# Optimization experiments

Hardware: AMD Instinct MI355X
Metric: run time of the kernel (lower is better)

## Reference

```python
import jax, jax.numpy as jnp
import numpy as np

D_MODEL = 1024
N_HEADS = 16
D_FF = 4096
B, T = 4, 2048
EPS = 1e-5


def layernorm(x, g, b):
    mu = jnp.mean(x, axis=-1, keepdims=True)
    var = jnp.var(x, axis=-1, keepdims=True)
    return (x - mu) * jax.lax.rsqrt(var + EPS) * g + b


def setup_inputs() -> dict:
    key = jax.random.key(0)
    ks = jax.random.split(key, 8)
    s = 0.02
    return {
        "x": jax.random.normal(ks[0], (B, T, D_MODEL), jnp.float32),
        "ln1_g": jnp.ones((D_MODEL,), jnp.float32),
        "ln1_b": jnp.zeros((D_MODEL,), jnp.float32),
        "wq": jax.random.normal(ks[1], (D_MODEL, D_MODEL), jnp.float32) * s,
        "bq": jnp.zeros((D_MODEL,), jnp.float32),
        "wk": jax.random.normal(ks[2], (D_MODEL, D_MODEL), jnp.float32) * s,
        "bk": jnp.zeros((D_MODEL,), jnp.float32),
        "wv": jax.random.normal(ks[3], (D_MODEL, D_MODEL), jnp.float32) * s,
        "bv": jnp.zeros((D_MODEL,), jnp.float32),
        "wo": jax.random.normal(ks[4], (D_MODEL, D_MODEL), jnp.float32) * s,
        "bo": jnp.zeros((D_MODEL,), jnp.float32),
        "ln2_g": jnp.ones((D_MODEL,), jnp.float32),
        "ln2_b": jnp.zeros((D_MODEL,), jnp.float32),
        "w1": jax.random.normal(ks[5], (D_FF, D_MODEL), jnp.float32) * s,
        "b1": jnp.zeros((D_FF,), jnp.float32),
        "w2": jax.random.normal(ks[6], (D_MODEL, D_FF), jnp.float32) * s,
        "b2": jnp.zeros((D_MODEL,), jnp.float32),
    }


def reference(x, ln1_g, ln1_b, wq, bq, wk, bk, wv, bv, wo, bo,
              ln2_g, ln2_b, w1, b1, w2, b2):
    d_k = D_MODEL // N_HEADS
    # --- attention sublayer (pre-LN) ---
    h = layernorm(x, ln1_g, ln1_b)                       # [B,T,D]
    q = (h @ wq.T + bq).reshape(B, T, N_HEADS, d_k)
    k = (h @ wk.T + bk).reshape(B, T, N_HEADS, d_k)
    v = (h @ wv.T + bv).reshape(B, T, N_HEADS, d_k)
    scores = jnp.einsum("bqhd,bkhd->bhqk", q, k) / jnp.sqrt(jnp.float32(d_k))
    attn = jax.nn.softmax(scores, axis=-1)               # [B,H,T,T]
    o = jnp.einsum("bhqk,bkhd->bqhd", attn, v).reshape(B, T, D_MODEL)
    x = x + (o @ wo.T + bo)
    # --- FFN sublayer ---
    h2 = layernorm(x, ln2_g, ln2_b)
    h2 = jax.nn.gelu(h2 @ w1.T + b1, approximate=False)  # torch GELU = exact erf
    x = x + (h2 @ w2.T + b2)
    return x
```

## Files before the change

### kernel.cpp

```cpp
#include <hip/hip_runtime.h>
#include <math.h>


#define D_MODEL 1024
#define D_FF    4096
#define NH      16
#define BATCH   4
#define SEQ     2048
#define DK      64
#define MTOK    (BATCH*SEQ)
#define NBH     (BATCH*NH)

typedef __bf16 bf16;
typedef _Float16 f16;
typedef bf16  bf16x4 __attribute__((ext_vector_type(4)));
typedef bf16  bf16x8 __attribute__((ext_vector_type(8)));
typedef f16   f16x4  __attribute__((ext_vector_type(4)));
typedef f16   f16x8  __attribute__((ext_vector_type(8)));
typedef __fp16 hf16x2 __attribute__((ext_vector_type(2)));
typedef __fp16 hf16x4 __attribute__((ext_vector_type(4)));
typedef __fp16 hf16x8 __attribute__((ext_vector_type(8)));
typedef float f32x4  __attribute__((ext_vector_type(4)));

__device__ __forceinline__ void gload_lds16(const void* g, void* l) {
  __builtin_amdgcn_global_load_lds(
      (__attribute__((address_space(1))) void*)g,
      (__attribute__((address_space(3))) void*)l, 16, 0, 0);
}

#define BAR() __builtin_amdgcn_s_barrier()
#define WAIT_VM0() do { asm volatile("s_waitcnt vmcnt(0)" ::: "memory"); \
  __builtin_amdgcn_sched_barrier(0); } while (0)

__device__ __forceinline__ float gelu_fast(float x) {
  float ax = fabsf(x) * 0.70710678118654752f;
  float t  = 1.0f / (1.0f + 0.3275911f * ax);
  float p  = t * (0.254829592f + t * (-0.284496736f + t * (1.421413741f +
             t * (-1.453152027f + t * 1.061405429f))));
  float e  = __builtin_amdgcn_exp2f(ax * ax * -1.4426950408889634f);
  float er = 1.0f - p * e;
  er = __builtin_copysignf(er, x);
  return 0.5f * x * (1.0f + er);
}

__global__ __launch_bounds__(256) void cast_w(const float* __restrict__ s,
                                              bf16* __restrict__ d, int n) {
  int i = (blockIdx.x * 256 + threadIdx.x) * 4;
  if (i >= n) return;
  float4 v = *(const float4*)(s + i);
  bf16x4 o;
  o[0] = (bf16)v.x; o[1] = (bf16)v.y; o[2] = (bf16)v.z; o[3] = (bf16)v.w;
  *(bf16x4*)(d + i) = o;
}

__global__ __launch_bounds__(256) void ln_kernel(const float* __restrict__ x,
                                                 const float* __restrict__ g,
                                                 const float* __restrict__ b,
                                                 bf16* __restrict__ out) {
  int row = blockIdx.x;
  int tid = threadIdx.x;
  const float* xr = x + (size_t)row * D_MODEL;
  float4 v = *(const float4*)(xr + tid * 4);
  float s  = v.x + v.y + v.z + v.w;
  float sq = v.x*v.x + v.y*v.y + v.z*v.z + v.w*v.w;
  #pragma unroll
  for (int off = 1; off < 64; off <<= 1) {
    s  += __shfl_xor(s,  off, 64);
    sq += __shfl_xor(sq, off, 64);
  }
  __shared__ float ls[4], lq[4];
  int wid = tid >> 6, lane = tid & 63;
  if (lane == 0) { ls[wid] = s; lq[wid] = sq; }
  __syncthreads();
  s  = ls[0] + ls[1] + ls[2] + ls[3];
  sq = lq[0] + lq[1] + lq[2] + lq[3];
  float mu   = s * (1.0f / D_MODEL);
  float var  = sq * (1.0f / D_MODEL) - mu * mu;
  float rstd = rsqrtf(var + 1e-5f);
  float4 gv = *(const float4*)(g + tid * 4);
  float4 bv = *(const float4*)(b + tid * 4);
  bf16x4 o;
  o[0] = (bf16)((v.x - mu) * rstd * gv.x + bv.x);
  o[1] = (bf16)((v.y - mu) * rstd * gv.y + bv.y);
  o[2] = (bf16)((v.z - mu) * rstd * gv.z + bv.z);
  o[3] = (bf16)((v.w - mu) * rstd * gv.w + bv.w);
  *(bf16x4*)(out + (size_t)row * D_MODEL + tid * 4) = o;
}

enum { EP_QKV = 0, EP_RESID = 1, EP_GELU = 2 };

#define QSCALE 0.18033688011112042f

template <int EP, int CFG>
__global__ __launch_bounds__(512) void gemm8p(
    const bf16* __restrict__ A, const bf16* __restrict__ W,
    const float* __restrict__ bias,
    const float* __restrict__ resid,
    float* __restrict__ out_f32,
    bf16* __restrict__ out_bf,
    int M, int N, int K) {
  constexpr int BM  = CFG ? 128 : 256;
  constexpr int BK  = CFG ? 64 : 32;
  constexpr int WM  = CFG ? 64 : 128;
  constexpr int FRN = WM / 16;
  constexpr int KKN = BK / 32;
  constexpr int RB  = BK * 2;
  constexpr int GR  = RB / 16;
  constexpr int RSH = CFG ? 7 : 6;
  constexpr int AB  = 16384;
  constexpr int TB  = AB + 256 * BK * 2;
  constexpr int L   = TB / 8192;

  __shared__ char lds[3 * TB];

  int tiles_n = N >> 8;
  int nwg = (M / BM) * tiles_n;
  int bid = blockIdx.x;
  int swz = (bid & 7) * (nwg >> 3) + (bid >> 3);
  int bm = swz / tiles_n, bn = swz % tiles_n;
  int m0 = bm * BM, n0 = bn << 8;
  int tid = threadIdx.x, wid = tid >> 6, lane = tid & 63;
  int wm = wid >> 2, wn = wid & 3;
  int l15 = lane & 15, l4 = lane >> 4;

  f32x4 acc[FRN][4];
  #pragma unroll
  for (int i = 0; i < FRN; i++)
    #pragma unroll
    for (int j = 0; j < 4; j++)
      #pragma unroll
      for (int e = 0; e < 4; e++) acc[i][j][e] = 0.f;

  auto STAGE = [&](int kt, int nb) {
    char* buf = lds + nb * TB;
    #pragma unroll
    for (int l = 0; l < L; ++l) {
      bool isA = l < 2;
      int o = (isA ? l : l - 2) * 8192 + tid * 16;
      int row = o >> RSH;
      int g = (o >> 4) & (GR - 1);
      int gs = g ^ (CFG ? (row & 7) : ((row >> 1) & 3));
      const bf16* src = (isA ? A + (size_t)(m0 + row) * K
                             : W + (size_t)(n0 + row) * K) + kt * BK + gs * 8;
      gload_lds16(src, buf + (isA ? 0 : AB) + o);
    }
  };

  int nt = K / BK;
  STAGE(0, 0);
  STAGE(1, 1);
  if constexpr (CFG) { asm volatile("s_waitcnt vmcnt(6)" ::: "memory"); }
  else               { asm volatile("s_waitcnt vmcnt(4)" ::: "memory"); }
  __builtin_amdgcn_sched_barrier(0);
  BAR();

  for (int t = 0; t < nt; ++t) {
    int cb = t % 3, nb = cb >= 1 ? cb - 1 : 2;
    const char* bc = lds + cb * TB;

    if (t + 2 < nt) STAGE(t + 2, nb);

    bf16x8 af[FRN][KKN], bfr[4][KKN];
    #pragma unroll
    for (int f = 0; f < FRN; ++f)
      #pragma unroll
      for (int kk = 0; kk < KKN; ++kk) {
        int row = wm * WM + f * 16 + l15;
        int g = (kk * 4 + l4) ^ (CFG ? (row & 7) : ((row >> 1) & 3));
        af[f][kk] = *(const bf16x8*)(bc + row * RB + g * 16);
      }
    #pragma unroll
    for (int fc = 0; fc < 4; ++fc)
      #pragma unroll
      for (int kk = 0; kk < KKN; ++kk) {
        int row = wn * 64 + fc * 16 + l15;
        int g = (kk * 4 + l4) ^ (CFG ? (row & 7) : ((row >> 1) & 3));
        bfr[fc][kk] = *(const bf16x8*)(bc + AB + row * RB + g * 16);
      }

    __builtin_amdgcn_s_setprio(1);
    #pragma unroll
    for (int f = 0; f < FRN; ++f)
      #pragma unroll
      for (int fc = 0; fc < 4; ++fc)
        #pragma unroll
        for (int kk = 0; kk < KKN; ++kk)
          acc[f][fc] = __builtin_amdgcn_mfma_f32_16x16x32_bf16(af[f][kk], bfr[fc][kk],
                                                               acc[f][fc], 0, 0, 0);
    __builtin_amdgcn_s_setprio(0);

    if (t + 2 < nt) {
      if constexpr (CFG) { asm volatile("s_waitcnt vmcnt(6)" ::: "memory"); }
      else               { asm volatile("s_waitcnt vmcnt(4)" ::: "memory"); }
      __builtin_amdgcn_sched_barrier(0);
    } else if (t + 1 < nt) {
      WAIT_VM0();
    }
    BAR();
  }

  if (EP == EP_QKV) {
    #pragma unroll
    for (int i = 0; i < FRN; i++)
      #pragma unroll
      for (int j = 0; j < 4; j++) {
        int gm0 = m0 + wm * WM + i * 16 + (l4 << 2);
        int gn  = n0 + wn * 64 + j * 16 + l15;
        int which = gn >> 10;
        int nn = gn & 1023, head = nn >> 6, d = nn & 63;
        int bb = gm0 >> 11, t = gm0 & 2047;
        float bv = bias[gn];
        if (which == 2) {
          int sbase = (t & ~31) + ((t >> 2) & 3) * 8 + ((t >> 4) & 1) * 4;
          f16x4 pk;
          #pragma unroll
          for (int jj = 0; jj < 4; jj++) pk[jj] = (f16)(acc[i][j][jj] + bv);
          *(f16x4*)((f16*)out_bf + (size_t)2 * NBH * SEQ * DK +
                    ((size_t)(bb * NH + head) * DK + d) * SEQ + sbase) = pk;
        } else {
          float scale = (which == 0) ? QSCALE : 1.0f;
          #pragma unroll
          for (int jj = 0; jj < 4; jj++) {
            float cv = (acc[i][j][jj] + bv) * scale;
            size_t idx = (size_t)which * (NBH * SEQ * DK) +
                         ((size_t)(bb * NH + head) * SEQ + (t + jj)) * DK + d;
            out_bf[idx] = (bf16)cv;
          }
        }
      }
  } else {
    #pragma unroll
    for (int i = 0; i < FRN; i++)
      #pragma unroll
      for (int j = 0; j < 4; j++)
        #pragma unroll
        for (int jj = 0; jj < 4; jj++) {
          int gm = m0 + wm * WM + i * 16 + (l4 << 2) + jj;
          int gn = n0 + wn * 64 + j * 16 + l15;
          float cv = acc[i][j][jj] + bias[gn];
          if (EP == EP_RESID) {
            size_t idx = (size_t)gm * N + gn;
            out_f32[idx] = resid[idx] + cv;
          } else {
            out_bf[(size_t)gm * N + gn] = (bf16)gelu_fast(cv);
          }
        }
  }
}

__global__ __launch_bounds__(512) void attn_kernel(
    const bf16* __restrict__ q, const bf16* __restrict__ k,
    const f16* __restrict__ vt, bf16* __restrict__ o) {
  __shared__ bf16 kt_lds[2][128 * 64];
  __shared__ f16  vt_lds[2][64 * 128];
  int bid = blockIdx.x;
  int swzb = (bid & 7) * 128 + (bid >> 3);
  int bh = swzb >> 4;
  int qt = swzb & 15;
  int t0 = qt << 7;
  int tid = threadIdx.x, wid = tid >> 6, lane = tid & 63;
  int l15 = lane & 15, l4 = lane >> 4;

  int kb0 = l15 * 128 + ((l4 ^ (l15 & 7)) << 4);
  int kb1 = l15 * 128 + (((4 + l4) ^ (l15 & 7)) << 4);
  int vb32[4];
  #pragma unroll
  for (int n = 0; n < 4; n++)
    vb32[n] = l15 * 256 + (((n * 4 + l4) ^ (l15 & 7)) << 4);

  const bf16* qbase = q + ((size_t)bh * SEQ + t0 + wid * 16 + l15) * DK;
  bf16x8 qf[2];
  qf[0] = *(const bf16x8*)(qbase + (l4 << 3));
  qf[1] = *(const bf16x8*)(qbase + 32 + (l4 << 3));

  f16x8 vones8;
  #pragma unroll
  for (int e = 0; e < 8; e++) vones8[e] = (f16)1.f;
  float m_run = -1e30f;
  f32x4 acc_o[4];
  f32x4 acc_l;
  #pragma unroll
  for (int nd = 0; nd < 4; nd++)
    #pragma unroll
    for (int e = 0; e < 4; e++) acc_o[nd][e] = 0.f;
  #pragma unroll
  for (int e = 0; e < 4; e++) acc_l[e] = 0.f;

  const bf16* gKsrc[2];
  const f16*  gVsrc[2];
  #pragma unroll
  for (int it = 0; it < 2; ++it) {
    int o = it * 8192 + tid * 16;
    int rowk = o >> 7, gk = (o >> 4) & 7;
    gKsrc[it] = k + ((size_t)bh * SEQ + rowk) * DK + ((gk ^ (rowk & 7)) << 3);
    int d = o >> 8, gd = (o >> 4) & 15;
    gVsrc[it] = vt + ((size_t)bh * DK + d) * SEQ + ((gd ^ (d & 7)) << 3);
  }

  auto stage = [&](int buf, int t) {
    int kv0 = t * 128;
    char* dK = (char*)&kt_lds[buf][0] + tid * 16;
    char* dV = (char*)&vt_lds[buf][0] + tid * 16;
    #pragma unroll
    for (int it = 0; it < 2; ++it) {
      gload_lds16(gKsrc[it] + (size_t)kv0 * DK, dK + it * 8192);
      gload_lds16(gVsrc[it] + kv0, dV + it * 8192);
    }
  };

  stage(0, 0);
  WAIT_VM0();
  BAR();

  for (int t = 0; t < SEQ / 128; ++t) {
    int cur = t & 1;
    if (t < SEQ / 128 - 1) stage(cur ^ 1, t + 1);
    const char* kbase = (const char*)&kt_lds[cur][0];
    const char* vbase = (const char*)&vt_lds[cur][0];

    f32x4 accs[8];
    #pragma unroll
    for (int n = 0; n < 8; n++)
      #pragma unroll
      for (int e = 0; e < 4; e++) accs[n][e] = 0.f;
    __builtin_amdgcn_s_setprio(1);
    #pragma unroll
    for (int n = 0; n < 8; n++) {
      bf16x8 kf0 = *(const bf16x8*)(kbase + kb0 + n * 2048);
      bf16x8 kf1 = *(const bf16x8*)(kbase + kb1 + n * 2048);
      accs[n] = __builtin_amdgcn_mfma_f32_16x16x32_bf16(kf0, qf[0], accs[n], 0, 0, 0);
      accs[n] = __builtin_amdgcn_mfma_f32_16x16x32_bf16(kf1, qf[1], accs[n], 0, 0, 0);
    }
    __builtin_amdgcn_s_setprio(0);

    float mloc = -1e30f;
    #pragma unroll
    for (int n = 0; n < 8; n++) {
      float a0 = fmaxf(accs[n][0], accs[n][1]);
      float a1 = fmaxf(accs[n][2], accs[n][3]);
      mloc = fmaxf(mloc, fmaxf(a0, a1));
    }
    float mt = fmaxf(mloc, __shfl_xor(mloc, 16, 64));
    mt = fmaxf(mt, __shfl_xor(mt, 32, 64));
    if (__any(mt > m_run + 8.0f)) {
      float mn = fmaxf(m_run, mt);
      float sc = __builtin_amdgcn_exp2f(m_run - mn);
      m_run = mn;
      float scr0 = __shfl(sc, l4 * 20 + 0, 64);
      float scr1 = __shfl(sc, l4 * 20 + 1, 64);
      float scr2 = __shfl(sc, l4 * 20 + 2, 64);
      float scr3 = __shfl(sc, l4 * 20 + 3, 64);
      #pragma unroll
      for (int nd = 0; nd < 4; nd++) {
        acc_o[nd][0] *= scr0; acc_o[nd][1] *= scr1;
        acc_o[nd][2] *= scr2; acc_o[nd][3] *= scr3;
      }
      acc_l[0] *= scr0; acc_l[1] *= scr1; acc_l[2] *= scr2; acc_l[3] *= scr3;
    }
    f16x8 pa32[4];
    #pragma unroll
    for (int n = 0; n < 4; n++) {
      float e0 = __builtin_amdgcn_exp2f(accs[2*n][0] - m_run);
      float e1 = __builtin_amdgcn_exp2f(accs[2*n][1] - m_run);
      float e2 = __builtin_amdgcn_exp2f(accs[2*n][2] - m_run);
      float e3 = __builtin_amdgcn_exp2f(accs[2*n][3] - m_run);
      float e4 = __builtin_amdgcn_exp2f(accs[2*n+1][0] - m_run);
      float e5 = __builtin_amdgcn_exp2f(accs[2*n+1][1] - m_run);
      float e6 = __builtin_amdgcn_exp2f(accs[2*n+1][2] - m_run);
      float e7 = __builtin_amdgcn_exp2f(accs[2*n+1][3] - m_run);
      hf16x2 p01 = __builtin_amdgcn_cvt_pkrtz(e0, e1);
      hf16x2 p23 = __builtin_amdgcn_cvt_pkrtz(e2, e3);
      hf16x2 p45 = __builtin_amdgcn_cvt_pkrtz(e4, e5);
      hf16x2 p67 = __builtin_amdgcn_cvt_pkrtz(e6, e7);
      hf16x4 lo = __builtin_shufflevector(p01, p23, 0, 1, 2, 3);
      hf16x4 hi = __builtin_shufflevector(p45, p67, 0, 1, 2, 3);
      hf16x8 cmb = __builtin_shufflevector(lo, hi, 0, 1, 2, 3, 4, 5, 6, 7);
      pa32[n] = __builtin_bit_cast(f16x8, cmb);
    }

    __builtin_amdgcn_s_setprio(1);
    #pragma unroll
    for (int n = 0; n < 4; n++) {
      #pragma unroll
      for (int nd = 0; nd < 4; nd++) {
        f16x8 vf = *(const f16x8*)(vbase + vb32[n] + nd * 4096);
        acc_o[nd] = __builtin_amdgcn_mfma_f32_16x16x32_f16(pa32[n], vf, acc_o[nd], 0, 0, 0);
      }
      acc_l = __builtin_amdgcn_mfma_f32_16x16x32_f16(pa32[n], vones8, acc_l, 0, 0, 0);
    }
    __builtin_amdgcn_s_setprio(0);

    if (t < SEQ / 128 - 1) { WAIT_VM0(); }
    BAR();
  }

  float rl0 = 1.0f / acc_l[0], rl1 = 1.0f / acc_l[1];
  float rl2 = 1.0f / acc_l[2], rl3 = 1.0f / acc_l[3];
  int bb = bh >> 4, hh = bh & 15;
  #pragma unroll
  for (int nd = 0; nd < 4; nd++) {
    int d = nd * 16 + l15;
    int rowb = t0 + wid * 16 + l4 * 4;
    o[((size_t)bb * SEQ + rowb + 0) * D_MODEL + hh * DK + d] = (bf16)(acc_o[nd][0] * rl0);
    o[((size_t)bb * SEQ + rowb + 1) * D_MODEL + hh * DK + d] = (bf16)(acc_o[nd][1] * rl1);
    o[((size_t)bb * SEQ + rowb + 2) * D_MODEL + hh * DK + d] = (bf16)(acc_o[nd][2] * rl2);
    o[((size_t)bb * SEQ + rowb + 3) * D_MODEL + hh * DK + d] = (bf16)(acc_o[nd][3] * rl3);
  }
}

extern "C" void kernel_launch(void* const* d_in, const int* in_sizes, int n_in,
                              void* d_out, int out_size, void* d_ws, size_t ws_size,
                              hipStream_t stream) {
  const float* x    = (const float*)d_in[0];
  const float* ln1g = (const float*)d_in[1];
  const float* ln1b = (const float*)d_in[2];
  const float* wq   = (const float*)d_in[3];
  const float* bq   = (const float*)d_in[4];
  const float* wk   = (const float*)d_in[5];
  const float* bk   = (const float*)d_in[6];
  const float* wv   = (const float*)d_in[7];
  const float* bv   = (const float*)d_in[8];
  const float* wo   = (const float*)d_in[9];
  const float* bo   = (const float*)d_in[10];
  const float* ln2g = (const float*)d_in[11];
  const float* ln2b = (const float*)d_in[12];
  const float* w1   = (const float*)d_in[13];
  const float* b1   = (const float*)d_in[14];
  const float* w2   = (const float*)d_in[15];
  const float* b2   = (const float*)d_in[16];
  float* out = (float*)d_out;

  char* ws = (char*)d_ws;
  bf16* wqkv_b = (bf16*)(ws);
  bf16* wo_b   = (bf16*)(ws + ((size_t)6  << 20));
  bf16* w1_b   = (bf16*)(ws + ((size_t)8  << 20));
  bf16* w2_b   = (bf16*)(ws + ((size_t)16 << 20));
  bf16* h_b    = (bf16*)(ws + ((size_t)24 << 20));
  bf16* qkv_b  = (bf16*)(ws + ((size_t)40 << 20));
  bf16* o_b    = (bf16*)(ws + ((size_t)88 << 20));
  bf16* ffn1_b = (bf16*)(ws + ((size_t)40 << 20));
  float* bqkv  = (float*)(ws + ((size_t)104 << 20));

  cast_w<<<1024, 256, 0, stream>>>(wq, wqkv_b, 1 << 20);
  cast_w<<<1024, 256, 0, stream>>>(wk, wqkv_b + (1 << 20), 1 << 20);
  cast_w<<<1024, 256, 0, stream>>>(wv, wqkv_b + (2 << 20), 1 << 20);
  cast_w<<<1024, 256, 0, stream>>>(wo, wo_b, 1 << 20);
  cast_w<<<4096, 256, 0, stream>>>(w1, w1_b, 1 << 22);
  cast_w<<<4096, 256, 0, stream>>>(w2, w2_b, 1 << 22);
  (void)hipMemcpyAsync(bqkv,        bq, 4096, hipMemcpyDeviceToDevice, stream);
  (void)hipMemcpyAsync(bqkv + 1024, bk, 4096, hipMemcpyDeviceToDevice, stream);
  (void)hipMemcpyAsync(bqkv + 2048, bv, 4096, hipMemcpyDeviceToDevice, stream);

  ln_kernel<<<MTOK, 256, 0, stream>>>(x, ln1g, ln1b, h_b);
  gemm8p<EP_QKV, 1><<<768, 512, 0, stream>>>(h_b, wqkv_b, bqkv, nullptr, nullptr,
                                             qkv_b, MTOK, 3072, 1024);
  attn_kernel<<<NBH * 16, 512, 0, stream>>>(qkv_b, qkv_b + (size_t)NBH * SEQ * DK,
                                            (const f16*)(qkv_b + (size_t)2 * NBH * SEQ * DK),
                                            o_b);
  gemm8p<EP_RESID, 1><<<256, 512, 0, stream>>>(o_b, wo_b, bo, x, out, nullptr,
                                               MTOK, 1024, 1024);
  ln_kernel<<<MTOK, 256, 0, stream>>>(out, ln2g, ln2b, h_b);
  gemm8p<EP_GELU, 0><<<512, 512, 0, stream>>>(h_b, w1_b, b1, nullptr, nullptr,
                                              ffn1_b, MTOK, 4096, 1024);
  gemm8p<EP_RESID, 1><<<256, 512, 0, stream>>>(ffn1_b, w2_b, b2, out, out, nullptr,
                                               MTOK, 1024, 4096);
}
```

Baseline: 410.6 us.

## Deepen GEMM prefetch to four buffers and halve attention KV tile

For the CFG=0 GEMM variant, the LDS ring grows from 3 to 4 buffers, so the prefetch distance becomes 3 tiles, with vmcnt waits adjusted to match. Separately, the attention kernel's K/V tile shrinks from 128 to 64 keys per iteration, halving its LDS footprint and per-iteration register use at the cost of twice as many barriers and online-softmax updates. The intent is to hide more global latency in the GEMM and raise occupancy in attention, but more LDS in the GEMM may lower its occupancy.

```diff
diff --git a/kernel.cpp b/kernel.cpp
--- a/kernel.cpp
+++ b/kernel.cpp
@@ -110,8 +110,10 @@
   constexpr int AB  = 16384;
   constexpr int TB  = AB + 256 * BK * 2;
   constexpr int L   = TB / 8192;
-
-  __shared__ char lds[3 * TB];
+  constexpr int NBUF = CFG ? 3 : 4;
+  constexpr int PD   = NBUF - 1;
+
+  __shared__ char lds[NBUF * TB];
 
   int tiles_n = N >> 8;
   int nwg = (M / BM) * tiles_n;
@@ -149,16 +151,19 @@
   int nt = K / BK;
   STAGE(0, 0);
   STAGE(1, 1);
-  if constexpr (CFG) { asm volatile("s_waitcnt vmcnt(6)" ::: "memory"); }
-  else               { asm volatile("s_waitcnt vmcnt(4)" ::: "memory"); }
+  if constexpr (CFG == 0) {
+    STAGE(2, 2);
+    asm volatile("s_waitcnt vmcnt(8)" ::: "memory");
+  } else {
+    asm volatile("s_waitcnt vmcnt(6)" ::: "memory");
+  }
   __builtin_amdgcn_sched_barrier(0);
   BAR();
 
   for (int t = 0; t < nt; ++t) {
-    int cb = t % 3, nb = cb >= 1 ? cb - 1 : 2;
-    const char* bc = lds + cb * TB;
-
-    if (t + 2 < nt) STAGE(t + 2, nb);
+    const char* bc = lds + (t % NBUF) * TB;
+
+    if (t + PD < nt) STAGE(t + PD, (t + PD) % NBUF);
 
     bf16x8 af[FRN][KKN], bfr[4][KKN];
     #pragma unroll
@@ -189,13 +194,15 @@
                                                                acc[f][fc], 0, 0, 0);
     __builtin_amdgcn_s_setprio(0);
 
-    if (t + 2 < nt) {
-      if constexpr (CFG) { asm volatile("s_waitcnt vmcnt(6)" ::: "memory"); }
-      else               { asm volatile("s_waitcnt vmcnt(4)" ::: "memory"); }
-      __builtin_amdgcn_sched_barrier(0);
-    } else if (t + 1 < nt) {
-      WAIT_VM0();
-    }
+    if constexpr (CFG == 0) {
+      if (t + 3 < nt)      { asm volatile("s_waitcnt vmcnt(8)" ::: "memory"); }
+      else if (t + 2 < nt) { asm volatile("s_waitcnt vmcnt(4)" ::: "memory"); }
+      else if (t + 1 < nt) { asm volatile("s_waitcnt vmcnt(0)" ::: "memory"); }
+    } else {
+      if (t + 2 < nt)      { asm volatile("s_waitcnt vmcnt(6)" ::: "memory"); }
+      else if (t + 1 < nt) { asm volatile("s_waitcnt vmcnt(0)" ::: "memory"); }
+    }
+    __builtin_amdgcn_sched_barrier(0);
     BAR();
   }
 
@@ -251,8 +258,8 @@
 __global__ __launch_bounds__(512) void attn_kernel(
     const bf16* __restrict__ q, const bf16* __restrict__ k,
     const f16* __restrict__ vt, bf16* __restrict__ o) {
-  __shared__ bf16 kt_lds[2][128 * 64];
-  __shared__ f16  vt_lds[2][64 * 128];
+  __shared__ bf16 kt_lds[2][64 * 64];
+  __shared__ f16  vt_lds[2][64 * 64];
   int bid = blockIdx.x;
   int swzb = (bid & 7) * 128 + (bid >> 3);
   int bh = swzb >> 4;
@@ -263,10 +270,10 @@
 
   int kb0 = l15 * 128 + ((l4 ^ (l15 & 7)) << 4);
   int kb1 = l15 * 128 + (((4 + l4) ^ (l15 & 7)) << 4);
-  int vb32[4];
-  #pragma unroll
-  for (int n = 0; n < 4; n++)
-    vb32[n] = l15 * 256 + (((n * 4 + l4) ^ (l15 & 7)) << 4);
+  int vb32[2];
+  #pragma unroll
+  for (int n = 0; n < 2; n++)
+    vb32[n] = l15 * 128 + (((n * 4 + l4) ^ (l15 & 7)) << 4);
 
   const bf16* qbase = q + ((size_t)bh * SEQ + t0 + wid * 16 + l15) * DK;
   bf16x8 qf[2];
@@ -286,46 +293,36 @@
   #pragma unroll
   for (int e = 0; e < 4; e++) acc_l[e] = 0.f;
 
-  const bf16* gKsrc[2];
-  const f16*  gVsrc[2];
-  #pragma unroll
-  for (int it = 0; it < 2; ++it) {
-    int o = it * 8192 + tid * 16;
-    int rowk = o >> 7, gk = (o >> 4) & 7;
-    gKsrc[it] = k + ((size_t)bh * SEQ + rowk) * DK + ((gk ^ (rowk & 7)) << 3);
-    int d = o >> 8, gd = (o >> 4) & 15;
-    gVsrc[it] = vt + ((size_t)bh * DK + d) * SEQ + ((gd ^ (d & 7)) << 3);
-  }
+  int oK = tid * 16;
+  int rowk = oK >> 7, gk = (oK >> 4) & 7;
+  const bf16* gKsrc = k + ((size_t)bh * SEQ + rowk) * DK + ((gk ^ (rowk & 7)) << 3);
+  int dV = oK >> 7, gd = (oK >> 4) & 7;
+  const f16* gVsrc = vt + ((size_t)bh * DK + dV) * SEQ + ((gd ^ (dV & 7)) << 3);
 
   auto stage = [&](int buf, int t) {
-    int kv0 = t * 128;
-    char* dK = (char*)&kt_lds[buf][0] + tid * 16;
-    char* dV = (char*)&vt_lds[buf][0] + tid * 16;
-    #pragma unroll
-    for (int it = 0; it < 2; ++it) {
-      gload_lds16(gKsrc[it] + (size_t)kv0 * DK, dK + it * 8192);
-      gload_lds16(gVsrc[it] + kv0, dV + it * 8192);
-    }
+    int kv0 = t * 64;
+    gload_lds16(gKsrc + (size_t)kv0 * DK, (char*)&kt_lds[buf][0] + tid * 16);
+    gload_lds16(gVsrc + kv0, (char*)&vt_lds[buf][0] + tid * 16);
   };
 
   stage(0, 0);
   WAIT_VM0();
   BAR();
 
-  for (int t = 0; t < SEQ / 128; ++t) {
+  for (int t = 0; t < SEQ / 64; ++t) {
     int cur = t & 1;
-    if (t < SEQ / 128 - 1) stage(cur ^ 1, t + 1);
+    if (t < SEQ / 64 - 1) stage(cur ^ 1, t + 1);
     const char* kbase = (const char*)&kt_lds[cur][0];
     const char* vbase = (const char*)&vt_lds[cur][0];
 
-    f32x4 accs[8];
-    #pragma unroll
-    for (int n = 0; n < 8; n++)
+    f32x4 accs[4];
+    #pragma unroll
+    for (int n = 0; n < 4; n++)
       #pragma unroll
       for (int e = 0; e < 4; e++) accs[n][e] = 0.f;
     __builtin_amdgcn_s_setprio(1);
     #pragma unroll
-    for (int n = 0; n < 8; n++) {
+    for (int n = 0; n < 4; n++) {
       bf16x8 kf0 = *(const bf16x8*)(kbase + kb0 + n * 2048);
       bf16x8 kf1 = *(const bf16x8*)(kbase + kb1 + n * 2048);
       accs[n] = __builtin_amdgcn_mfma_f32_16x16x32_bf16(kf0, qf[0], accs[n], 0, 0, 0);
@@ -335,7 +332,7 @@
 
     float mloc = -1e30f;
     #pragma unroll
-    for (int n = 0; n < 8; n++) {
+    for (int n = 0; n < 4; n++) {
       float a0 = fmaxf(accs[n][0], accs[n][1]);
       float a1 = fmaxf(accs[n][2], accs[n][3]);
       mloc = fmaxf(mloc, fmaxf(a0, a1));
@@ -357,9 +354,9 @@
       }
       acc_l[0] *= scr0; acc_l[1] *= scr1; acc_l[2] *= scr2; acc_l[3] *= scr3;
     }
-    f16x8 pa32[4];
-    #pragma unroll
-    for (int n = 0; n < 4; n++) {
+    f16x8 pa32[2];
+    #pragma unroll
+    for (int n = 0; n < 2; n++) {
       float e0 = __builtin_amdgcn_exp2f(accs[2*n][0] - m_run);
       float e1 = __builtin_amdgcn_exp2f(accs[2*n][1] - m_run);
       float e2 = __builtin_amdgcn_exp2f(accs[2*n][2] - m_run);
@@ -380,17 +377,17 @@
 
     __builtin_amdgcn_s_setprio(1);
     #pragma unroll
-    for (int n = 0; n < 4; n++) {
+    for (int n = 0; n < 2; n++) {
       #pragma unroll
       for (int nd = 0; nd < 4; nd++) {
-        f16x8 vf = *(const f16x8*)(vbase + vb32[n] + nd * 4096);
+        f16x8 vf = *(const f16x8*)(vbase + vb32[n] + nd * 2048);
         acc_o[nd] = __builtin_amdgcn_mfma_f32_16x16x32_f16(pa32[n], vf, acc_o[nd], 0, 0, 0);
       }
       acc_l = __builtin_amdgcn_mfma_f32_16x16x32_f16(pa32[n], vones8, acc_l, 0, 0, 0);
     }
     __builtin_amdgcn_s_setprio(0);
 
-    if (t < SEQ / 128 - 1) { WAIT_VM0(); }
+    if (t < SEQ / 64 - 1) { WAIT_VM0(); }
     BAR();
   }
 
```

After: 413.3 us. About the same (+0.7%).
